# Kernel optimization log

Measured on AMD Instinct MI355X. Metric: run time of the kernel, lower is better.

## Reference

```python
import jax, jax.numpy as jnp
import numpy as np

B, A, H, D, K = 131072, 6, 256, 128, 512
BETA = 0.25
VQ_LOSS_WEIGHT = 1.0


def setup_inputs() -> dict:
    key = jax.random.key(0)
    ks = jax.random.split(key, 16)
    s = 0.05
    inp = {
        "action": jax.random.normal(ks[0], (B, A), jnp.float32),
        # encoder: Linear(A,H)+ReLU, Linear(H,H)+ReLU, Linear(H,D)
        "enc1_w": jax.random.normal(ks[1], (H, A), jnp.float32) * s,
        "enc1_b": jnp.zeros((H,), jnp.float32),
        "enc2_w": jax.random.normal(ks[2], (H, H), jnp.float32) * s,
        "enc2_b": jnp.zeros((H,), jnp.float32),
        "mu_w": jax.random.normal(ks[3], (D, H), jnp.float32) * s,
        "mu_b": jnp.zeros((D,), jnp.float32),
        # VQ codebook, uniform(-1/K, 1/K) as in torch init
        "emb": jax.random.uniform(ks[4], (K, D), jnp.float32, -1.0 / K, 1.0 / K),
        # decoder: Linear(D,H)+ReLU, Linear(H,H)+ReLU, Linear(H,A)+Tanh
        "dec1_w": jax.random.normal(ks[5], (H, D), jnp.float32) * s,
        "dec1_b": jnp.zeros((H,), jnp.float32),
        "dec2_w": jax.random.normal(ks[6], (H, H), jnp.float32) * s,
        "dec2_b": jnp.zeros((H,), jnp.float32),
        "rec_w": jax.random.normal(ks[7], (A, H), jnp.float32) * s,
        "rec_b": jnp.zeros((A,), jnp.float32),
    }
    return inp


def _lin(x, w, b):
    return x @ w.T + b


def reference(action, enc1_w, enc1_b, enc2_w, enc2_b, mu_w, mu_b, emb,
              dec1_w, dec1_b, dec2_w, dec2_b, rec_w, rec_b):
    sg = jax.lax.stop_gradient
    # encoder MLP -> (B, D)
    h = jax.nn.relu(_lin(action, enc1_w, enc1_b))
    h = jax.nn.relu(_lin(h, enc2_w, enc2_b))
    enc = _lin(h, mu_w, mu_b)
    # VQ: argmin over squared L2 distance (same argmin as torch.cdist p=2)
    d2 = (jnp.sum(enc * enc, axis=1, keepdims=True)
          - 2.0 * (enc @ emb.T)
          + jnp.sum(emb * emb, axis=1))  # (B, K)
    idx = jnp.argmin(d2, axis=-1)  # (B,)
    q = emb[idx]  # (B, D) gather == onehot @ emb
    commitment_loss = jnp.mean((enc - sg(q)) ** 2)
    embedding_loss = jnp.mean((q - sg(enc)) ** 2)
    vq_loss = BETA * commitment_loss + embedding_loss
    # straight-through estimator
    q_st = enc + sg(q - enc)
    # decoder MLP (decode_action_head + decode_common + recons_action_head)
    h = jax.nn.relu(_lin(q_st, dec1_w, dec1_b))
    h = jax.nn.relu(_lin(h, dec2_w, dec2_b))
    recons = jnp.tanh(_lin(h, rec_w, rec_b))
    recons_loss = jnp.mean((recons - action) ** 2)
    total_loss = recons_loss + VQ_LOSS_WEIGHT * vq_loss
    return idx, q_st, total_loss
```

## Files before the change

### kernel.cpp

```cpp
#include <hip/hip_runtime.h>
#include <hip/hip_bf16.h>

#define NB 131072
#define MARGINF 5e-7f
#define WS_E2 256
#define WS_MASK 768
#define WS_MASKW 4096
#define WS_BASE_BYTES ((768 + 4096) * 4)
#define WS_SPLIT_F 4864
#define OFF_W2 0
#define OFF_W3 131072
#define OFF_EMB 196608
#define OFF_D1 327680
#define OFF_D2 393216
#define OFF_RW 524288
#define SPLIT_TOTAL 532480

typedef __attribute__((ext_vector_type(8))) short short8v;
typedef __attribute__((ext_vector_type(4))) float f32x4;
typedef __attribute__((ext_vector_type(4))) unsigned short ushort4v;

#define SWC(j) ((((j) >> 2) & 7) << 2)

__device__ __forceinline__ unsigned short bf16rn(float x) {
    unsigned u = __float_as_uint(x);
    unsigned r = u + 0x7fffu + ((u >> 16) & 1u);
    return (unsigned short)(r >> 16);
}
__device__ __forceinline__ void split2(float x, unsigned short& h, unsigned short& l) {
    h = bf16rn(x);
    float hf = __uint_as_float((unsigned)h << 16);
    l = bf16rn(x - hf);
}

__global__ void prep_kernel(
    const float* __restrict__ w2, const float* __restrict__ w3,
    const float* __restrict__ emb, const float* __restrict__ d1w,
    const float* __restrict__ d2w, const float* __restrict__ rw,
    float* __restrict__ ws, int do_splits)
{
    const int total = 512 + 266240;
    unsigned short* wsb = (unsigned short*)(ws + WS_SPLIT_F);
    for (int idx = blockIdx.x * 256 + threadIdx.x; idx < total; idx += gridDim.x * 256) {
        if (idx < 512) {
            const float* e = emb + (size_t)idx * 128;
            float s0 = 0.f, s1 = 0.f, s2 = 0.f, s3 = 0.f;
            for (int d = 0; d < 128; d += 4) {
                s0 += e[d] * e[d];     s1 += e[d + 1] * e[d + 1];
                s2 += e[d + 2] * e[d + 2]; s3 += e[d + 3] * e[d + 3];
            }
            ws[WS_E2 + idx] = (s0 + s1) + (s2 + s3);
            continue;
        }
        if (!do_splits) continue;
        int j = idx - 512;
        int base, K, o, k;
        float src;
        if (j < 65536) {
            o = j >> 8; k = j & 255; base = OFF_W2; K = 256; src = w2[o * 256 + k];
        } else if (j < 98304) {
            j -= 65536; o = j >> 8; k = j & 255; base = OFF_W3; K = 256; src = w3[o * 256 + k];
        } else if (j < 163840) {
            j -= 98304; o = j >> 7; k = j & 127; base = OFF_EMB; K = 128; src = emb[o * 128 + k];
        } else if (j < 196608) {
            j -= 163840; o = j >> 7; k = j & 127; base = OFF_D1; K = 128; src = d1w[o * 128 + k];
        } else if (j < 262144) {
            j -= 196608; o = j >> 8; k = j & 255; base = OFF_D2; K = 256; src = d2w[o * 256 + k];
        } else {
            j -= 262144; o = j >> 8; k = j & 255; base = OFF_RW; K = 256;
            src = (o < 6) ? rw[o * 256 + k] : 0.f;
        }
        unsigned short h, l;
        split2(src, h, l);
        int jt = o >> 4, c = k >> 5;
        int lane = (((k >> 3) & 3) << 4) | (o & 15);
        int e = k & 7;
        int a = base + ((jt * (K >> 5) + c) * 2) * 512 + lane * 8 + e;
        wsb[a] = h;
        wsb[a + 512] = l;
    }
}


template<int NJT, int KC, bool RELU, bool SQSUM, int TERMS, bool WRITELO>
__device__ __forceinline__ void mfma_mlp4(
    const short8v* __restrict__ Wf, const float* __restrict__ bias,
    unsigned short* HHp, unsigned short* HLp, float* ENC2Wp,
    int w, int lane)
{
    const int lc = lane & 15, lg = lane >> 4;
    f32x4 acc[NJT][4];
#pragma unroll
    for (int jj = 0; jj < NJT; ++jj)
#pragma unroll
        for (int rt = 0; rt < 4; ++rt)
            acc[jj][rt] = (f32x4){0.f, 0.f, 0.f, 0.f};

    __syncthreads();
    for (int c = 0; c < KC; ++c) {
        const int boff = c * 32 + lg * 8;
        short8v bh[4], bl[4];
#pragma unroll
        for (int rt = 0; rt < 4; ++rt) {
            bh[rt] = *(const short8v*)&HHp[(rt * 16 + lc) * 264 + boff];
            if (TERMS == 3)
                bl[rt] = *(const short8v*)&HLp[(rt * 16 + lc) * 264 + boff];
        }
#pragma unroll
        for (int jj = 0; jj < NJT; ++jj) {
            int fi = (((w * NJT + jj) * KC + c) * 2) * 64 + lane;
            short8v ah = Wf[fi];
            if (TERMS == 3) {
                short8v al = Wf[fi + 64];
#pragma unroll
                for (int rt = 0; rt < 4; ++rt) {
                    acc[jj][rt] = __builtin_amdgcn_mfma_f32_16x16x32_bf16(al, bh[rt], acc[jj][rt], 0, 0, 0);
                    acc[jj][rt] = __builtin_amdgcn_mfma_f32_16x16x32_bf16(ah, bl[rt], acc[jj][rt], 0, 0, 0);
                    acc[jj][rt] = __builtin_amdgcn_mfma_f32_16x16x32_bf16(ah, bh[rt], acc[jj][rt], 0, 0, 0);
                }
            } else {
#pragma unroll
                for (int rt = 0; rt < 4; ++rt)
                    acc[jj][rt] = __builtin_amdgcn_mfma_f32_16x16x32_bf16(ah, bh[rt], acc[jj][rt], 0, 0, 0);
            }
        }
    }
    __syncthreads();

    float sq[4] = {0.f, 0.f, 0.f, 0.f};
#pragma unroll
    for (int jj = 0; jj < NJT; ++jj) {
        int j0 = (w * NJT + jj) * 16 + lg * 4;
        float4 bv = *(const float4*)&bias[j0];
        float bb[4] = {bv.x, bv.y, bv.z, bv.w};
#pragma unroll
        for (int rt = 0; rt < 4; ++rt) {
            int r = rt * 16 + lc;
            ushort4v hv, lv;
#pragma unroll
            for (int reg = 0; reg < 4; ++reg) {
                float v = acc[jj][rt][reg] + bb[reg];
                if (RELU) v = fmaxf(v, 0.f);
                if (SQSUM) sq[rt] += v * v;
                if (WRITELO) {
                    unsigned short h, l;
                    split2(v, h, l);
                    hv[reg] = h; lv[reg] = l;
                } else {
                    hv[reg] = bf16rn(v);
                }
            }
            *(ushort4v*)&HHp[r * 264 + j0] = hv;
            if (WRITELO) *(ushort4v*)&HLp[r * 264 + j0] = lv;
        }
    }
    if (SQSUM) {
#pragma unroll
        for (int rt = 0; rt < 4; ++rt) {
            float s = sq[rt];
            s += __shfl_xor(s, 16);
            s += __shfl_xor(s, 32);
            if (lg == 0) ENC2Wp[w * 64 + rt * 16 + lc] = s;
        }
    }
}

__global__ __launch_bounds__(256, 2) void vqvae_main_mfma(
    const float* __restrict__ action,
    const float* __restrict__ w1, const float* __restrict__ b1,
    const float* __restrict__ b2, const float* __restrict__ b3,
    const float* __restrict__ emb,
    const float* __restrict__ d1b, const float* __restrict__ d2b,
    const float* __restrict__ rb,
    float* __restrict__ out, float* __restrict__ ws)
{
    extern __shared__ __align__(16) unsigned short DYN[];
    unsigned short* HH = DYN;
    unsigned short* HL = DYN + 64 * 264;

    __shared__ float AT[64 * 6];
    __shared__ float E2S[512];
    __shared__ float TOPV[4][64][3];
    __shared__ float ENC2W[4 * 64];
    __shared__ int IDXR[64];
    __shared__ int FLAGR[64];
    __shared__ float RED[8];

    const int t = threadIdx.x;
    const int w = t >> 6, lane = t & 63;
    const int lc = lane & 15, lg = lane >> 4;
    const int row0 = blockIdx.x * 64;
    const unsigned short* wsb = (const unsigned short*)(ws + WS_SPLIT_F);
    const short8v* W2f = (const short8v*)wsb + OFF_W2 / 8;
    const short8v* W3f = (const short8v*)wsb + OFF_W3 / 8;
    const short8v* EMBf = (const short8v*)wsb + OFF_EMB / 8;
    const short8v* D1f = (const short8v*)wsb + OFF_D1 / 8;
    const short8v* D2f = (const short8v*)wsb + OFF_D2 / 8;
    const short8v* RWf = (const short8v*)wsb + OFF_RW / 8;

    for (int i = t; i < 384; i += 256) AT[i] = action[(size_t)row0 * 6 + i];
    for (int i = t; i < 512; i += 256) E2S[i] = ws[WS_E2 + i];
    __syncthreads();

    {
        float wr[6];
#pragma unroll
        for (int i = 0; i < 6; ++i) wr[i] = w1[t * 6 + i];
        float bb = b1[t];
        for (int r = 0; r < 64; ++r) {
            float s = bb;
#pragma unroll
            for (int i = 0; i < 6; ++i) s += wr[i] * AT[r * 6 + i];
            s = fmaxf(s, 0.f);
            unsigned short h, l;
            split2(s, h, l);
            HH[r * 264 + t] = h;
            HL[r * 264 + t] = l;
        }
    }

    mfma_mlp4<4, 8, true, false, 3, true>(W2f, b2, HH, HL, ENC2W, w, lane);
    mfma_mlp4<2, 8, false, true, 3, true>(W3f, b3, HH, HL, ENC2W, w, lane);

    float lvq = 0.f, lrec = 0.f;
    {
        float v1[4][4], v2[4][4];
        int k1r[4][4];
#pragma unroll
        for (int rt = 0; rt < 4; ++rt)
#pragma unroll
            for (int reg = 0; reg < 4; ++reg) {
                v1[rt][reg] = 1e30f; v2[rt][reg] = 1e30f; k1r[rt][reg] = 0;
            }
        __syncthreads();
#pragma unroll
        for (int p = 0; p < 2; ++p) {
            f32x4 vacc[4][4];
#pragma unroll
            for (int kt = 0; kt < 4; ++kt)
#pragma unroll
                for (int rt = 0; rt < 4; ++rt)
                    vacc[kt][rt] = (f32x4){0.f, 0.f, 0.f, 0.f};
            for (int c = 0; c < 4; ++c) {
                const int aoff = c * 32 + lg * 8;
                short8v ah[4], al[4];
#pragma unroll
                for (int rt = 0; rt < 4; ++rt) {
                    ah[rt] = *(const short8v*)&HH[(rt * 16 + lc) * 264 + aoff];
                    al[rt] = *(const short8v*)&HL[(rt * 16 + lc) * 264 + aoff];
                }
#pragma unroll
                for (int kt = 0; kt < 4; ++kt) {
                    int ktg = w * 8 + p * 4 + kt;
                    int fi = ((ktg * 4 + c) * 2) * 64 + lane;
                    short8v bh = EMBf[fi];
                    short8v bl = EMBf[fi + 64];
#pragma unroll
                    for (int rt = 0; rt < 4; ++rt) {
                        vacc[kt][rt] = __builtin_amdgcn_mfma_f32_16x16x32_bf16(al[rt], bh, vacc[kt][rt], 0, 0, 0);
                        vacc[kt][rt] = __builtin_amdgcn_mfma_f32_16x16x32_bf16(ah[rt], bl, vacc[kt][rt], 0, 0, 0);
                        vacc[kt][rt] = __builtin_amdgcn_mfma_f32_16x16x32_bf16(ah[rt], bh, vacc[kt][rt], 0, 0, 0);
                    }
                }
            }
#pragma unroll
            for (int kt = 0; kt < 4; ++kt) {
                int k = (w * 8 + p * 4 + kt) * 16 + lc;
                float ek = E2S[k];
#pragma unroll
                for (int rt = 0; rt < 4; ++rt)
#pragma unroll
                    for (int reg = 0; reg < 4; ++reg) {
                        float dd = ek - 2.f * vacc[kt][rt][reg];
                        if (dd < v1[rt][reg]) {
                            v2[rt][reg] = v1[rt][reg]; v1[rt][reg] = dd; k1r[rt][reg] = k;
                        } else if (dd < v2[rt][reg]) v2[rt][reg] = dd;
                    }
            }
        }
        __syncthreads();

#pragma unroll
        for (int m = 1; m < 16; m <<= 1) {
#pragma unroll
            for (int rt = 0; rt < 4; ++rt)
#pragma unroll
                for (int reg = 0; reg < 4; ++reg) {
                    float ov1 = __shfl_xor(v1[rt][reg], m);
                    int ok1 = __shfl_xor(k1r[rt][reg], m);
                    float ov2 = __shfl_xor(v2[rt][reg], m);
                    if (ov1 < v1[rt][reg] ||
                        (ov1 == v1[rt][reg] && ok1 < k1r[rt][reg])) {
                        v2[rt][reg] = fminf(v1[rt][reg], ov2);
                        v1[rt][reg] = ov1; k1r[rt][reg] = ok1;
                    } else {
                        v2[rt][reg] = fminf(v2[rt][reg], ov1);
                    }
                }
        }
        if (lc == 0) {
#pragma unroll
            for (int rt = 0; rt < 4; ++rt)
#pragma unroll
                for (int reg = 0; reg < 4; ++reg) {
                    int row = rt * 16 + lg * 4 + reg;
                    TOPV[w][row][0] = v1[rt][reg];
                    TOPV[w][row][1] = __int_as_float(k1r[rt][reg]);
                    TOPV[w][row][2] = v2[rt][reg];
                }
        }
    }
    __syncthreads();

    if (t < 64) {
        float v1 = 1e30f, v2 = 1e30f; int k1 = 0;
#pragma unroll
        for (int ww = 0; ww < 4; ++ww) {
            float ov1 = TOPV[ww][t][0];
            int ok1 = __float_as_int(TOPV[ww][t][1]);
            float ov2 = TOPV[ww][t][2];
            if (ov1 < v1 || (ov1 == v1 && ok1 < k1)) {
                v2 = fminf(v1, ov2); v1 = ov1; k1 = ok1;
            } else {
                v2 = fminf(v2, ov1);
            }
        }
        int flag = (v2 - v1 >= MARGINF) ? 0 : 1;
        IDXR[t] = k1;
        FLAGR[t] = flag;
        int row = row0 + t;
        if (flag)
            atomicOr((unsigned int*)ws + WS_MASK + (row >> 5), 1u << (row & 31));
        out[row] = (float)k1;
        if (!flag) {
            float enc2 = ENC2W[0 * 64 + t] + ENC2W[1 * 64 + t] +
                         ENC2W[2 * 64 + t] + ENC2W[3 * 64 + t];
            lvq = enc2 + v1;
        }
    }
    __syncthreads();

    {
        int d = t & 127, rhalf = t >> 7;
#pragma unroll
        for (int e = 0; e < 32; ++e) {
            int r = (e << 1) | rhalf;
            int k1 = IDXR[r];
            float q = emb[(size_t)k1 * 128 + d];
            out[NB + (size_t)(row0 + r) * 128 + d] = q;
            HH[r * 264 + d] = bf16rn(q);
        }
    }

    mfma_mlp4<4, 4, true, false, 1, false>(D1f, d1b, HH, HL, ENC2W, w, lane);
    mfma_mlp4<4, 8, true, false, 1, false>(D2f, d2b, HH, HL, ENC2W, w, lane);
    __syncthreads();

    {
        f32x4 racc = (f32x4){0.f, 0.f, 0.f, 0.f};
        for (int c = 0; c < 8; ++c) {
            const int boff = c * 32 + lg * 8;
            short8v bh = *(const short8v*)&HH[(w * 16 + lc) * 264 + boff];
            int fi = (c * 2) * 64 + lane;
            short8v ah = RWf[fi];
            racc = __builtin_amdgcn_mfma_f32_16x16x32_bf16(ah, bh, racc, 0, 0, 0);
        }
        int r = w * 16 + lc;
#pragma unroll
        for (int reg = 0; reg < 4; ++reg) {
            int j = lg * 4 + reg;
            if (j < 6) {
                float rec = tanhf(racc[reg] + rb[j]);
                float df = rec - AT[r * 6 + j];
                if (!FLAGR[r]) lrec += df * df;
            }
        }
    }

#pragma unroll
    for (int m = 1; m < 64; m <<= 1) {
        lvq += __shfl_xor(lvq, m);
        lrec += __shfl_xor(lrec, m);
    }
    if ((t & 63) == 0) { RED[t >> 6] = lvq; RED[4 + (t >> 6)] = lrec; }
    __syncthreads();
    if (t == 0) {
        int slot = blockIdx.x & 63;
        atomicAdd((double*)ws + slot, (double)((RED[0] + RED[1]) + (RED[2] + RED[3])));
        atomicAdd((double*)ws + 64 + slot, (double)((RED[4] + RED[5]) + (RED[6] + RED[7])));
    }
}

__global__ __launch_bounds__(256) void vqvae_fix(
    const float* __restrict__ action,
    const float* __restrict__ w1, const float* __restrict__ b1,
    const float* __restrict__ w2, const float* __restrict__ b2,
    const float* __restrict__ w3, const float* __restrict__ b3,
    const float* __restrict__ emb,
    const float* __restrict__ d1w, const float* __restrict__ d1b,
    const float* __restrict__ d2w, const float* __restrict__ d2b,
    const float* __restrict__ rw, const float* __restrict__ rb,
    float* __restrict__ out, float* __restrict__ ws)
{
    __shared__ double H1[256];
    __shared__ double H2[256];
    __shared__ double ENC[128];
    __shared__ double QD[128];
    __shared__ double SRED[256];
    __shared__ int SK[256];
    __shared__ double SA[6];

    const int t = threadIdx.x;

    for (int widx = blockIdx.x; widx < WS_MASKW; widx += gridDim.x) {
        const unsigned int word = ((const unsigned int*)ws)[WS_MASK + widx];
        if (word == 0u) continue;

        for (int bit = 0; bit < 32; ++bit) {
            if (!(word & (1u << bit))) continue;
            const int row = (widx << 5) + bit;

            if (t < 6) SA[t] = (double)action[(size_t)row * 6 + t];
            __syncthreads();
            {
                double a = (double)b1[t];
#pragma unroll
                for (int i = 0; i < 6; ++i) a += (double)w1[t * 6 + i] * SA[i];
                H1[t] = a > 0.0 ? a : 0.0;
            }
            __syncthreads();
            {
                const float* w = w2 + (size_t)t * 256;
                double a0 = 0, a1 = 0, a2 = 0, a3 = 0;
                for (int i = 0; i < 256; i += 4) {
                    a0 += (double)w[i] * H1[i];     a1 += (double)w[i + 1] * H1[i + 1];
                    a2 += (double)w[i + 2] * H1[i + 2]; a3 += (double)w[i + 3] * H1[i + 3];
                }
                double a = (double)b2[t] + a0 + a1 + a2 + a3;
                H2[t] = a > 0.0 ? a : 0.0;
            }
            __syncthreads();
            if (t < 128) {
                const float* w = w3 + (size_t)t * 256;
                double a0 = 0, a1 = 0, a2 = 0, a3 = 0;
                for (int i = 0; i < 256; i += 4) {
                    a0 += (double)w[i] * H2[i];     a1 += (double)w[i + 1] * H2[i + 1];
                    a2 += (double)w[i + 2] * H2[i + 2]; a3 += (double)w[i + 3] * H2[i + 3];
                }
                ENC[t] = (double)b3[t] + a0 + a1 + a2 + a3;
            }
            __syncthreads();
            double best = 1e300; int bk = 0;
#pragma unroll
            for (int kk = 0; kk < 2; ++kk) {
                int k = t + kk * 256;
                const float* e = emb + (size_t)k * 128;
                double s0 = 0, s1 = 0;
                for (int d = 0; d < 128; d += 2) {
                    double df0 = ENC[d] - (double)e[d];
                    double df1 = ENC[d + 1] - (double)e[d + 1];
                    s0 += df0 * df0; s1 += df1 * df1;
                }
                double s = s0 + s1;
                if (s < best) { best = s; bk = k; }
            }
            SRED[t] = best; SK[t] = bk;
            __syncthreads();
            for (int st = 128; st > 0; st >>= 1) {
                if (t < st) {
                    double ov = SRED[t + st]; int ok = SK[t + st];
                    if (ov < SRED[t] || (ov == SRED[t] && ok < SK[t])) { SRED[t] = ov; SK[t] = ok; }
                }
                __syncthreads();
            }
            const int bestk = SK[0];
            double lv = 0.0;
            if (t < 128) {
                double q = (double)emb[(size_t)bestk * 128 + t];
                QD[t] = q;
                double df = ENC[t] - q;
                lv = df * df;
                out[NB + (size_t)row * 128 + t] = (float)q;
            }
            if (t == 0) out[row] = (float)bestk;
            __syncthreads();
            {
                const float* w = d1w + (size_t)t * 128;
                double a0 = 0, a1 = 0;
                for (int i = 0; i < 128; i += 2) {
                    a0 += (double)w[i] * QD[i]; a1 += (double)w[i + 1] * QD[i + 1];
                }
                double a = (double)d1b[t] + a0 + a1;
                H1[t] = a > 0.0 ? a : 0.0;
            }
            __syncthreads();
            {
                const float* w = d2w + (size_t)t * 256;
                double a0 = 0, a1 = 0, a2 = 0, a3 = 0;
                for (int i = 0; i < 256; i += 4) {
                    a0 += (double)w[i] * H1[i];     a1 += (double)w[i + 1] * H1[i + 1];
                    a2 += (double)w[i + 2] * H1[i + 2]; a3 += (double)w[i + 3] * H1[i + 3];
                }
                double a = (double)d2b[t] + a0 + a1 + a2 + a3;
                H2[t] = a > 0.0 ? a : 0.0;
            }
            __syncthreads();
            double lr = 0.0;
            if (t < 6) {
                const float* w = rw + (size_t)t * 256;
                double a0 = 0, a1 = 0;
                for (int i = 0; i < 256; i += 2) {
                    a0 += (double)w[i] * H2[i]; a1 += (double)w[i + 1] * H2[i + 1];
                }
                double rec = tanh((double)rb[t] + a0 + a1);
                double df = rec - SA[t];
                lr = df * df;
            }
            SRED[t] = lv;
            __syncthreads();
            for (int st = 128; st > 0; st >>= 1) {
                if (t < st) SRED[t] += SRED[t + st];
                __syncthreads();
            }
            if (t == 0) atomicAdd((double*)ws + 0, SRED[0]);
            if (t < 6) atomicAdd((double*)ws + 64, lr);
            __syncthreads();
        }
    }
}

__global__ void vqvae_fin(const float* __restrict__ ws, float* __restrict__ out) {
    if (threadIdx.x == 0 && blockIdx.x == 0) {
        const double* D = (const double*)ws;
        double sv = 0.0, sr = 0.0;
        for (int i = 0; i < 64; ++i) { sv += D[i]; sr += D[64 + i]; }
        double loss = sr / ((double)NB * 6.0) + 1.25 * (sv / ((double)NB * 128.0));
        out[(size_t)NB * 129] = (float)loss;
    }
}

static __device__ __forceinline__ void gemm_out256(
    const float* __restrict__ W, const float* __restrict__ bias, int IN,
    const float* __restrict__ hin, float* __restrict__ hout,
    float* __restrict__ WC, int t, int tx, int r0, bool do_relu)
{
    float acc[2][4][4];
#pragma unroll
    for (int g = 0; g < 2; ++g)
#pragma unroll
        for (int a = 0; a < 4; ++a)
#pragma unroll
            for (int b = 0; b < 4; ++b) acc[g][a][b] = 0.f;
    float4 pa = *(const float4*)(W + (size_t)t * IN);
    float4 pb = *(const float4*)(W + (size_t)t * IN + 4);
    for (int i0 = 0; i0 < IN; i0 += 8) {
        __syncthreads();
        WC[0 * 256 + t] = pa.x; WC[1 * 256 + t] = pa.y;
        WC[2 * 256 + t] = pa.z; WC[3 * 256 + t] = pa.w;
        WC[4 * 256 + t] = pb.x; WC[5 * 256 + t] = pb.y;
        WC[6 * 256 + t] = pb.z; WC[7 * 256 + t] = pb.w;
        __syncthreads();
        if (i0 + 8 < IN) {
            pa = *(const float4*)(W + (size_t)t * IN + i0 + 8);
            pb = *(const float4*)(W + (size_t)t * IN + i0 + 12);
        }
#pragma unroll
        for (int i = 0; i < 8; ++i) {
            int row = i0 + i;
            float4 h = *(const float4*)&hin[row * 32 + (r0 ^ SWC(row))];
            float4 w0 = *(const float4*)&WC[i * 256 + 4 * tx];
            float4 w1v = *(const float4*)&WC[i * 256 + 128 + 4 * tx];
            float wv0[4] = {w0.x, w0.y, w0.z, w0.w};
            float wv1[4] = {w1v.x, w1v.y, w1v.z, w1v.w};
            float hv[4] = {h.x, h.y, h.z, h.w};
#pragma unroll
            for (int a = 0; a < 4; ++a)
#pragma unroll
                for (int b = 0; b < 4; ++b) {
                    acc[0][a][b] += wv0[a] * hv[b];
                    acc[1][a][b] += wv1[a] * hv[b];
                }
        }
    }
#pragma unroll
    for (int g = 0; g < 2; ++g)
#pragma unroll
        for (int a = 0; a < 4; ++a) {
            int j = g * 128 + 4 * tx + a;
            float bj = bias[j];
            float4 v;
            v.x = acc[g][a][0] + bj; v.y = acc[g][a][1] + bj;
            v.z = acc[g][a][2] + bj; v.w = acc[g][a][3] + bj;
            if (do_relu) {
                v.x = fmaxf(v.x, 0.f); v.y = fmaxf(v.y, 0.f);
                v.z = fmaxf(v.z, 0.f); v.w = fmaxf(v.w, 0.f);
            }
            *(float4*)&hout[j * 32 + (r0 ^ SWC(j))] = v;
        }
    __syncthreads();
}

__global__ __launch_bounds__(256, 2) void vqvae_main_fp32(
    const float* __restrict__ action,
    const float* __restrict__ w1, const float* __restrict__ b1,
    const float* __restrict__ w2, const float* __restrict__ b2,
    const float* __restrict__ w3, const float* __restrict__ b3,
    const float* __restrict__ emb,
    const float* __restrict__ d1w, const float* __restrict__ d1b,
    const float* __restrict__ d2w, const float* __restrict__ d2b,
    const float* __restrict__ rw, const float* __restrict__ rb,
    float* __restrict__ out, float* __restrict__ ws)
{
    __shared__ float X[256 * 32];
    __shared__ float Y[256 * 32];
    __shared__ float WC[2048];
    __shared__ float AT[6 * 32];
    __shared__ int IDXR[32];
    __shared__ int FLAGR[32];
    __shared__ float RED[8];

    const int t = threadIdx.x;
    const int tx = t & 31, ty = t >> 5;
    const int r0 = ty * 4;
    const int row0 = blockIdx.x * 32;

    if (t < 192) {
        int r = t / 6, i = t - r * 6;
        AT[i * 32 + r] = action[(size_t)row0 * 6 + t];
    }
    __syncthreads();
    {
#pragma unroll
        for (int i = 0; i < 6; ++i) WC[i * 256 + t] = w1[t * 6 + i];
        __syncthreads();
        float acc[2][4][4];
#pragma unroll
        for (int g = 0; g < 2; ++g)
#pragma unroll
            for (int a = 0; a < 4; ++a)
#pragma unroll
                for (int b = 0; b < 4; ++b) acc[g][a][b] = 0.f;
#pragma unroll
        for (int i = 0; i < 6; ++i) {
            float4 h = *(const float4*)&AT[i * 32 + r0];
            float4 w0 = *(const float4*)&WC[i * 256 + 4 * tx];
            float4 w1v = *(const float4*)&WC[i * 256 + 128 + 4 * tx];
            float wv0[4] = {w0.x, w0.y, w0.z, w0.w};
            float wv1[4] = {w1v.x, w1v.y, w1v.z, w1v.w};
            float hv[4] = {h.x, h.y, h.z, h.w};
#pragma unroll
            for (int a = 0; a < 4; ++a)
#pragma unroll
                for (int b = 0; b < 4; ++b) {
                    acc[0][a][b] += wv0[a] * hv[b];
                    acc[1][a][b] += wv1[a] * hv[b];
                }
        }
#pragma unroll
        for (int g = 0; g < 2; ++g)
#pragma unroll
            for (int a = 0; a < 4; ++a) {
                int j = g * 128 + 4 * tx + a;
                float bj = b1[j];
                float4 v;
                v.x = fmaxf(acc[g][a][0] + bj, 0.f);
                v.y = fmaxf(acc[g][a][1] + bj, 0.f);
                v.z = fmaxf(acc[g][a][2] + bj, 0.f);
                v.w = fmaxf(acc[g][a][3] + bj, 0.f);
                *(float4*)&X[j * 32 + (r0 ^ SWC(j))] = v;
            }
        __syncthreads();
    }
    gemm_out256(w2, b2, 256, X, Y, WC, t, tx, r0, true);
    {
        float acc[4][4];
#pragma unroll
        for (int a = 0; a < 4; ++a)
#pragma unroll
            for (int b = 0; b < 4; ++b) acc[a][b] = 0.f;
        float4 pa, pb;
        if (t < 128) {
            pa = *(const float4*)(w3 + (size_t)t * 256);
            pb = *(const float4*)(w3 + (size_t)t * 256 + 4);
        }
        for (int i0 = 0; i0 < 256; i0 += 8) {
            __syncthreads();
            if (t < 128) {
                WC[0 * 128 + t] = pa.x; WC[1 * 128 + t] = pa.y;
                WC[2 * 128 + t] = pa.z; WC[3 * 128 + t] = pa.w;
                WC[4 * 128 + t] = pb.x; WC[5 * 128 + t] = pb.y;
                WC[6 * 128 + t] = pb.z; WC[7 * 128 + t] = pb.w;
            }
            __syncthreads();
            if (t < 128 && i0 + 8 < 256) {
                pa = *(const float4*)(w3 + (size_t)t * 256 + i0 + 8);
                pb = *(const float4*)(w3 + (size_t)t * 256 + i0 + 12);
            }
#pragma unroll
            for (int i = 0; i < 8; ++i) {
                int row = i0 + i;
                float4 h = *(const float4*)&Y[row * 32 + (r0 ^ SWC(row))];
                float4 w0 = *(const float4*)&WC[i * 128 + 4 * tx];
                float wv[4] = {w0.x, w0.y, w0.z, w0.w};
                float hv[4] = {h.x, h.y, h.z, h.w};
#pragma unroll
                for (int a = 0; a < 4; ++a)
#pragma unroll
                    for (int b = 0; b < 4; ++b) acc[a][b] += wv[a] * hv[b];
            }
        }
#pragma unroll
        for (int a = 0; a < 4; ++a) {
            int j = 4 * tx + a;
            float bj = b3[j];
            float4 v;
            v.x = acc[a][0] + bj; v.y = acc[a][1] + bj;
            v.z = acc[a][2] + bj; v.w = acc[a][3] + bj;
            *(float4*)&X[j * 32 + (r0 ^ SWC(j))] = v;
        }
        __syncthreads();
    }
    {
        float bv1[4], bv2[4];
        int bk1[4];
        float acc[4][4][4];
#pragma unroll
        for (int p = 0; p < 4; ++p)
#pragma unroll
            for (int a = 0; a < 4; ++a)
#pragma unroll
                for (int b = 0; b < 4; ++b) acc[p][a][b] = 0.f;
        float4 qa = *(const float4*)(emb + (size_t)t * 128);
        float4 qb = *(const float4*)(emb + (size_t)(t + 256) * 128);
        for (int d0 = 0; d0 < 128; d0 += 4) {
            __syncthreads();
            WC[0 * 512 + t] = qa.x; WC[1 * 512 + t] = qa.y;
            WC[2 * 512 + t] = qa.z; WC[3 * 512 + t] = qa.w;
            WC[0 * 512 + 256 + t] = qb.x; WC[1 * 512 + 256 + t] = qb.y;
            WC[2 * 512 + 256 + t] = qb.z; WC[3 * 512 + 256 + t] = qb.w;
            __syncthreads();
            if (d0 + 4 < 128) {
                qa = *(const float4*)(emb + (size_t)t * 128 + d0 + 4);
                qb = *(const float4*)(emb + (size_t)(t + 256) * 128 + d0 + 4);
            }
#pragma unroll
            for (int i = 0; i < 4; ++i) {
                int row = d0 + i;
                float4 h = *(const float4*)&X[row * 32 + (r0 ^ SWC(row))];
                float hv[4] = {h.x, h.y, h.z, h.w};
#pragma unroll
                for (int p = 0; p < 4; ++p) {
                    float4 w0 = *(const float4*)&WC[i * 512 + p * 128 + 4 * tx];
                    float wv[4] = {w0.x, w0.y, w0.z, w0.w};
#pragma unroll
                    for (int a = 0; a < 4; ++a)
#pragma unroll
                        for (int b = 0; b < 4; ++b) acc[p][a][b] += wv[a] * hv[b];
                }
            }
        }
#pragma unroll
        for (int b = 0; b < 4; ++b) { bv1[b] = 1e30f; bv2[b] = 1e30f; bk1[b] = 0; }
#pragma unroll
        for (int p = 0; p < 4; ++p)
#pragma unroll
            for (int a = 0; a < 4; ++a) {
                int k = p * 128 + 4 * tx + a;
                float ek = ws[WS_E2 + k];
#pragma unroll
                for (int b = 0; b < 4; ++b) {
                    float dd = ek - 2.f * acc[p][a][b];
                    if (dd < bv1[b]) { bv2[b] = bv1[b]; bv1[b] = dd; bk1[b] = k; }
                    else if (dd < bv2[b]) bv2[b] = dd;
                }
            }
#pragma unroll
        for (int m = 1; m < 32; m <<= 1) {
#pragma unroll
            for (int b = 0; b < 4; ++b) {
                float ov1 = __shfl_xor(bv1[b], m);
                int ok1 = __shfl_xor(bk1[b], m);
                float ov2 = __shfl_xor(bv2[b], m);
                if (ov1 < bv1[b] || (ov1 == bv1[b] && ok1 < bk1[b])) {
                    bv2[b] = fminf(bv1[b], ov2);
                    bv1[b] = ov1; bk1[b] = ok1;
                } else {
                    bv2[b] = fminf(bv2[b], ov1);
                }
            }
        }
        if (tx == 0) {
#pragma unroll
            for (int b = 0; b < 4; ++b) {
                IDXR[r0 + b] = bk1[b];
                FLAGR[r0 + b] = (bv2[b] - bv1[b] >= MARGINF) ? 0 : 1;
            }
        }
    }
    __syncthreads();
    if (t < 32) {
        int row = row0 + t;
        if (FLAGR[t])
            atomicOr((unsigned int*)ws + WS_MASK + (row >> 5), 1u << (row & 31));
        out[row] = (float)IDXR[t];
    }
    float lvq = 0.f, lrec = 0.f;
    {
        int d = t & 127, rq = t >> 7;
        int cd = SWC(d);
#pragma unroll
        for (int e = 0; e < 4; ++e) {
            int rr = (rq + 2 * e) * 4;
            float4 en = *(const float4*)&X[d * 32 + (rr ^ cd)];
            float q0 = emb[(size_t)IDXR[rr + 0] * 128 + d];
            float q1 = emb[(size_t)IDXR[rr + 1] * 128 + d];
            float q2 = emb[(size_t)IDXR[rr + 2] * 128 + d];
            float q3 = emb[(size_t)IDXR[rr + 3] * 128 + d];
            float4 qv; qv.x = q0; qv.y = q1; qv.z = q2; qv.w = q3;
            *(float4*)&X[(128 + d) * 32 + (rr ^ cd)] = qv;
            if (!FLAGR[rr + 0]) lvq += (en.x - q0) * (en.x - q0);
            if (!FLAGR[rr + 1]) lvq += (en.y - q1) * (en.y - q1);
            if (!FLAGR[rr + 2]) lvq += (en.z - q2) * (en.z - q2);
            if (!FLAGR[rr + 3]) lvq += (en.w - q3) * (en.w - q3);
            out[NB + (size_t)(row0 + rr + 0) * 128 + d] = q0;
            out[NB + (size_t)(row0 + rr + 1) * 128 + d] = q1;
            out[NB + (size_t)(row0 + rr + 2) * 128 + d] = q2;
            out[NB + (size_t)(row0 + rr + 3) * 128 + d] = q3;
        }
    }
    __syncthreads();
    gemm_out256(d1w, d1b, 128, X + 128 * 32, Y, WC, t, tx, r0, true);
    gemm_out256(d2w, d2b, 256, Y, X, WC, t, tx, r0, true);
    if (t < 192) {
        int jj = t >> 5, r = t & 31;
        const float* wr = rw + jj * 256;
        float a0 = 0.f, a1 = 0.f, a2 = 0.f, a3 = 0.f;
        for (int i = 0; i < 256; i += 4) {
            a0 += wr[i] * X[i * 32 + (r ^ SWC(i))];
            a1 += wr[i + 1] * X[(i + 1) * 32 + (r ^ SWC(i + 1))];
            a2 += wr[i + 2] * X[(i + 2) * 32 + (r ^ SWC(i + 2))];
            a3 += wr[i + 3] * X[(i + 3) * 32 + (r ^ SWC(i + 3))];
        }
        float rec = tanhf(rb[jj] + (a0 + a1) + (a2 + a3));
        float df = rec - AT[jj * 32 + r];
        if (!FLAGR[r]) lrec = df * df;
    }
#pragma unroll
    for (int m = 1; m < 64; m <<= 1) {
        lvq += __shfl_xor(lvq, m);
        lrec += __shfl_xor(lrec, m);
    }
    if ((t & 63) == 0) { RED[t >> 6] = lvq; RED[4 + (t >> 6)] = lrec; }
    __syncthreads();
    if (t == 0) {
        int slot = blockIdx.x & 63;
        atomicAdd((double*)ws + slot, (double)((RED[0] + RED[1]) + (RED[2] + RED[3])));
        atomicAdd((double*)ws + 64 + slot, (double)((RED[4] + RED[5]) + (RED[6] + RED[7])));
    }
}

extern "C" void kernel_launch(void* const* d_in, const int* in_sizes, int n_in,
                              void* d_out, int out_size, void* d_ws, size_t ws_size,
                              hipStream_t stream) {
    const float* action = (const float*)d_in[0];
    const float* w1 = (const float*)d_in[1];
    const float* b1 = (const float*)d_in[2];
    const float* w2 = (const float*)d_in[3];
    const float* b2 = (const float*)d_in[4];
    const float* w3 = (const float*)d_in[5];
    const float* b3 = (const float*)d_in[6];
    const float* emb = (const float*)d_in[7];
    const float* d1w = (const float*)d_in[8];
    const float* d1b = (const float*)d_in[9];
    const float* d2w = (const float*)d_in[10];
    const float* d2b = (const float*)d_in[11];
    const float* rw = (const float*)d_in[12];
    const float* rb = (const float*)d_in[13];
    float* out = (float*)d_out;
    float* ws = (float*)d_ws;

    const size_t need_mfma = (size_t)WS_BASE_BYTES + (size_t)SPLIT_TOTAL * 2;
    const int use_mfma = (ws_size >= need_mfma) ? 1 : 0;
    const int dyn_lds = 64 * 264 * 2 * 2;

    size_t clear = ws_size < (size_t)WS_BASE_BYTES ? ws_size : (size_t)WS_BASE_BYTES;
    hipMemsetAsync(d_ws, 0, clear, stream);

    prep_kernel<<<1043, 256, 0, stream>>>(w2, w3, emb, d1w, d2w, rw, ws, use_mfma);
    if (use_mfma) {
        hipFuncSetAttribute((const void*)vqvae_main_mfma,
                            hipFuncAttributeMaxDynamicSharedMemorySize, dyn_lds);
        vqvae_main_mfma<<<NB / 64, 256, dyn_lds, stream>>>(action, w1, b1, b2, b3, emb,
                                                           d1b, d2b, rb, out, ws);
    } else {
        vqvae_main_fp32<<<NB / 32, 256, 0, stream>>>(action, w1, b1, w2, b2, w3, b3, emb,
                                                     d1w, d1b, d2w, d2b, rw, rb, out, ws);
    }
    vqvae_fix<<<256, 256, 0, stream>>>(action, w1, b1, w2, b2, w3, b3, emb,
                                       d1w, d1b, d2w, d2b, rw, rb, out, ws);
    vqvae_fin<<<1, 64, 0, stream>>>(ws, out);
}
```

Baseline: 395.6 us.

## Use single-bf16 VQ distance screening with exact fp32 candidate rescoring

Replaces the 3-term split-bf16 MFMA distance computation with a single bf16 hi*hi pass. Each row takes a coarse minimum, and every code within a margin of it is marked as a candidate in an LDS bitmask. Candidates are then rescored exactly in fp32 by one thread per row, which yields the argmin and the second-best margin. It also drops the low-half weight writes for matrices that no longer need them and moves the workspace clearing from a memset into the prep kernel. The gain is a third of the MFMA work in the VQ stage, paid for with serial per-row rescoring whose cost grows with the candidate count, plus an accuracy risk if the coarse margin is too tight.

```diff
diff --git a/kernel.cpp b/kernel.cpp
--- a/kernel.cpp
+++ b/kernel.cpp
@@ -3,6 +3,7 @@
 
 #define NB 131072
 #define MARGINF 5e-7f
+#define CMARGINF 4e-4f
 #define WS_E2 256
 #define WS_MASK 768
 #define WS_MASKW 4096
@@ -39,9 +40,15 @@
     const float* __restrict__ d2w, const float* __restrict__ rw,
     float* __restrict__ ws, int do_splits)
 {
+    const int gid = blockIdx.x * 256 + threadIdx.x;
+    const int stride = gridDim.x * 256;
+    for (int z = gid; z < 4352; z += stride) {
+        int a = (z < 256) ? z : (512 + z);
+        ws[a] = 0.f;
+    }
     const int total = 512 + 266240;
     unsigned short* wsb = (unsigned short*)(ws + WS_SPLIT_F);
-    for (int idx = blockIdx.x * 256 + threadIdx.x; idx < total; idx += gridDim.x * 256) {
+    for (int idx = gid; idx < total; idx += stride) {
         if (idx < 512) {
             const float* e = emb + (size_t)idx * 128;
             float s0 = 0.f, s1 = 0.f, s2 = 0.f, s3 = 0.f;
@@ -56,19 +63,20 @@
         int j = idx - 512;
         int base, K, o, k;
         float src;
+        bool wlo;
         if (j < 65536) {
-            o = j >> 8; k = j & 255; base = OFF_W2; K = 256; src = w2[o * 256 + k];
+            o = j >> 8; k = j & 255; base = OFF_W2; K = 256; src = w2[o * 256 + k]; wlo = true;
         } else if (j < 98304) {
-            j -= 65536; o = j >> 8; k = j & 255; base = OFF_W3; K = 256; src = w3[o * 256 + k];
+            j -= 65536; o = j >> 8; k = j & 255; base = OFF_W3; K = 256; src = w3[o * 256 + k]; wlo = true;
         } else if (j < 163840) {
-            j -= 98304; o = j >> 7; k = j & 127; base = OFF_EMB; K = 128; src = emb[o * 128 + k];
+            j -= 98304; o = j >> 7; k = j & 127; base = OFF_EMB; K = 128; src = emb[o * 128 + k]; wlo = false;
         } else if (j < 196608) {
-            j -= 163840; o = j >> 7; k = j & 127; base = OFF_D1; K = 128; src = d1w[o * 128 + k];
+            j -= 163840; o = j >> 7; k = j & 127; base = OFF_D1; K = 128; src = d1w[o * 128 + k]; wlo = false;
         } else if (j < 262144) {
-            j -= 196608; o = j >> 8; k = j & 255; base = OFF_D2; K = 256; src = d2w[o * 256 + k];
+            j -= 196608; o = j >> 8; k = j & 255; base = OFF_D2; K = 256; src = d2w[o * 256 + k]; wlo = false;
         } else {
             j -= 262144; o = j >> 8; k = j & 255; base = OFF_RW; K = 256;
-            src = (o < 6) ? rw[o * 256 + k] : 0.f;
+            src = (o < 6) ? rw[o * 256 + k] : 0.f; wlo = false;
         }
         unsigned short h, l;
         split2(src, h, l);
@@ -77,7 +85,7 @@
         int e = k & 7;
         int a = base + ((jt * (K >> 5) + c) * 2) * 512 + lane * 8 + e;
         wsb[a] = h;
-        wsb[a + 512] = l;
+        if (wlo) wsb[a + 512] = l;
     }
 }
 
@@ -180,8 +188,10 @@
 
     __shared__ float AT[64 * 6];
     __shared__ float E2S[512];
-    __shared__ float TOPV[4][64][3];
     __shared__ float ENC2W[4 * 64];
+    __shared__ float WMIN[4][64];
+    __shared__ float CMIN[64];
+    __shared__ unsigned int CAND[64 * 16];
     __shared__ int IDXR[64];
     __shared__ int FLAGR[64];
     __shared__ float RED[8];
@@ -224,117 +234,114 @@
 
     float lvq = 0.f, lrec = 0.f;
     {
-        float v1[4][4], v2[4][4];
-        int k1r[4][4];
+        for (int i = t; i < 1024; i += 256) CAND[i] = 0u;
+        f32x4 vacc[8][4];
+#pragma unroll
+        for (int kt = 0; kt < 8; ++kt)
+#pragma unroll
+            for (int rt = 0; rt < 4; ++rt)
+                vacc[kt][rt] = (f32x4){0.f, 0.f, 0.f, 0.f};
+        __syncthreads();
+        for (int c = 0; c < 4; ++c) {
+            const int aoff = c * 32 + lg * 8;
+            short8v ah[4];
+#pragma unroll
+            for (int rt = 0; rt < 4; ++rt)
+                ah[rt] = *(const short8v*)&HH[(rt * 16 + lc) * 264 + aoff];
+#pragma unroll
+            for (int kt = 0; kt < 8; ++kt) {
+                int fi = (((w * 8 + kt) * 4 + c) * 2) * 64 + lane;
+                short8v bh = EMBf[fi];
+#pragma unroll
+                for (int rt = 0; rt < 4; ++rt)
+                    vacc[kt][rt] = __builtin_amdgcn_mfma_f32_16x16x32_bf16(ah[rt], bh, vacc[kt][rt], 0, 0, 0);
+            }
+        }
+        float v1[4][4];
 #pragma unroll
         for (int rt = 0; rt < 4; ++rt)
 #pragma unroll
-            for (int reg = 0; reg < 4; ++reg) {
-                v1[rt][reg] = 1e30f; v2[rt][reg] = 1e30f; k1r[rt][reg] = 0;
-            }
+            for (int reg = 0; reg < 4; ++reg) v1[rt][reg] = 1e30f;
+#pragma unroll
+        for (int kt = 0; kt < 8; ++kt) {
+            int k = (w * 8 + kt) * 16 + lc;
+            float ek = E2S[k];
+#pragma unroll
+            for (int rt = 0; rt < 4; ++rt)
+#pragma unroll
+                for (int reg = 0; reg < 4; ++reg) {
+                    float dd = ek - 2.f * vacc[kt][rt][reg];
+                    v1[rt][reg] = fminf(v1[rt][reg], dd);
+                }
+        }
+#pragma unroll
+        for (int m = 1; m < 16; m <<= 1)
+#pragma unroll
+            for (int rt = 0; rt < 4; ++rt)
+#pragma unroll
+                for (int reg = 0; reg < 4; ++reg)
+                    v1[rt][reg] = fminf(v1[rt][reg], __shfl_xor(v1[rt][reg], m));
+        if (lc == 0) {
+#pragma unroll
+            for (int rt = 0; rt < 4; ++rt)
+#pragma unroll
+                for (int reg = 0; reg < 4; ++reg)
+                    WMIN[w][rt * 16 + lg * 4 + reg] = v1[rt][reg];
+        }
         __syncthreads();
-#pragma unroll
-        for (int p = 0; p < 2; ++p) {
-            f32x4 vacc[4][4];
-#pragma unroll
-            for (int kt = 0; kt < 4; ++kt)
-#pragma unroll
-                for (int rt = 0; rt < 4; ++rt)
-                    vacc[kt][rt] = (f32x4){0.f, 0.f, 0.f, 0.f};
-            for (int c = 0; c < 4; ++c) {
-                const int aoff = c * 32 + lg * 8;
-                short8v ah[4], al[4];
-#pragma unroll
-                for (int rt = 0; rt < 4; ++rt) {
-                    ah[rt] = *(const short8v*)&HH[(rt * 16 + lc) * 264 + aoff];
-                    al[rt] = *(const short8v*)&HL[(rt * 16 + lc) * 264 + aoff];
-                }
-#pragma unroll
-                for (int kt = 0; kt < 4; ++kt) {
-                    int ktg = w * 8 + p * 4 + kt;
-                    int fi = ((ktg * 4 + c) * 2) * 64 + lane;
-                    short8v bh = EMBf[fi];
-                    short8v bl = EMBf[fi + 64];
-#pragma unroll
-                    for (int rt = 0; rt < 4; ++rt) {
-                        vacc[kt][rt] = __builtin_amdgcn_mfma_f32_16x16x32_bf16(al[rt], bh, vacc[kt][rt], 0, 0, 0);
-                        vacc[kt][rt] = __builtin_amdgcn_mfma_f32_16x16x32_bf16(ah[rt], bl, vacc[kt][rt], 0, 0, 0);
-                        vacc[kt][rt] = __builtin_amdgcn_mfma_f32_16x16x32_bf16(ah[rt], bh, vacc[kt][rt], 0, 0, 0);
-                    }
-                }
-            }
-#pragma unroll
-            for (int kt = 0; kt < 4; ++kt) {
-                int k = (w * 8 + p * 4 + kt) * 16 + lc;
-                float ek = E2S[k];
-#pragma unroll
-                for (int rt = 0; rt < 4; ++rt)
-#pragma unroll
-                    for (int reg = 0; reg < 4; ++reg) {
-                        float dd = ek - 2.f * vacc[kt][rt][reg];
-                        if (dd < v1[rt][reg]) {
-                            v2[rt][reg] = v1[rt][reg]; v1[rt][reg] = dd; k1r[rt][reg] = k;
-                        } else if (dd < v2[rt][reg]) v2[rt][reg] = dd;
-                    }
-            }
-        }
+        if (t < 64)
+            CMIN[t] = fminf(fminf(WMIN[0][t], WMIN[1][t]), fminf(WMIN[2][t], WMIN[3][t]));
         __syncthreads();
-
-#pragma unroll
-        for (int m = 1; m < 16; m <<= 1) {
-#pragma unroll
-            for (int rt = 0; rt < 4; ++rt)
-#pragma unroll
-                for (int reg = 0; reg < 4; ++reg) {
-                    float ov1 = __shfl_xor(v1[rt][reg], m);
-                    int ok1 = __shfl_xor(k1r[rt][reg], m);
-                    float ov2 = __shfl_xor(v2[rt][reg], m);
-                    if (ov1 < v1[rt][reg] ||
-                        (ov1 == v1[rt][reg] && ok1 < k1r[rt][reg])) {
-                        v2[rt][reg] = fminf(v1[rt][reg], ov2);
-                        v1[rt][reg] = ov1; k1r[rt][reg] = ok1;
-                    } else {
-                        v2[rt][reg] = fminf(v2[rt][reg], ov1);
-                    }
-                }
-        }
-        if (lc == 0) {
+#pragma unroll
+        for (int kt = 0; kt < 8; ++kt) {
+            int k = (w * 8 + kt) * 16 + lc;
+            float ek = E2S[k];
 #pragma unroll
             for (int rt = 0; rt < 4; ++rt)
 #pragma unroll
                 for (int reg = 0; reg < 4; ++reg) {
                     int row = rt * 16 + lg * 4 + reg;
-                    TOPV[w][row][0] = v1[rt][reg];
-                    TOPV[w][row][1] = __int_as_float(k1r[rt][reg]);
-                    TOPV[w][row][2] = v2[rt][reg];
+                    float dd = ek - 2.f * vacc[kt][rt][reg];
+                    if (!(dd > CMIN[row] + CMARGINF))
+                        atomicOr(&CAND[row * 16 + (k >> 5)], 1u << (k & 31));
                 }
         }
     }
     __syncthreads();
 
     if (t < 64) {
+        const int row = t;
         float v1 = 1e30f, v2 = 1e30f; int k1 = 0;
-#pragma unroll
-        for (int ww = 0; ww < 4; ++ww) {
-            float ov1 = TOPV[ww][t][0];
-            int ok1 = __float_as_int(TOPV[ww][t][1]);
-            float ov2 = TOPV[ww][t][2];
-            if (ov1 < v1 || (ov1 == v1 && ok1 < k1)) {
-                v2 = fminf(v1, ov2); v1 = ov1; k1 = ok1;
-            } else {
-                v2 = fminf(v2, ov1);
+        for (int wd = 0; wd < 16; ++wd) {
+            unsigned int m = CAND[row * 16 + wd];
+            while (m) {
+                int b = __ffs(m) - 1; m &= m - 1;
+                int k = wd * 32 + b;
+                const float* ek = emb + (size_t)k * 128;
+                float s0 = 0.f, s1 = 0.f;
+                for (int d = 0; d < 128; d += 2) {
+                    float e0 = __uint_as_float((unsigned)HH[row * 264 + d] << 16)
+                             + __uint_as_float((unsigned)HL[row * 264 + d] << 16);
+                    float e1 = __uint_as_float((unsigned)HH[row * 264 + d + 1] << 16)
+                             + __uint_as_float((unsigned)HL[row * 264 + d + 1] << 16);
+                    s0 += e0 * ek[d];
+                    s1 += e1 * ek[d + 1];
+                }
+                float dd = E2S[k] - 2.f * (s0 + s1);
+                if (dd < v1) { v2 = v1; v1 = dd; k1 = k; }
+                else if (dd < v2) v2 = dd;
             }
         }
         int flag = (v2 - v1 >= MARGINF) ? 0 : 1;
-        IDXR[t] = k1;
-        FLAGR[t] = flag;
-        int row = row0 + t;
+        IDXR[row] = k1;
+        FLAGR[row] = flag;
+        int grow = row0 + row;
         if (flag)
-            atomicOr((unsigned int*)ws + WS_MASK + (row >> 5), 1u << (row & 31));
-        out[row] = (float)k1;
+            atomicOr((unsigned int*)ws + WS_MASK + (grow >> 5), 1u << (grow & 31));
+        out[grow] = (float)k1;
         if (!flag) {
-            float enc2 = ENC2W[0 * 64 + t] + ENC2W[1 * 64 + t] +
-                         ENC2W[2 * 64 + t] + ENC2W[3 * 64 + t];
+            float enc2 = ENC2W[0 * 64 + row] + ENC2W[1 * 64 + row] +
+                         ENC2W[2 * 64 + row] + ENC2W[3 * 64 + row];
             lvq = enc2 + v1;
         }
     }
@@ -883,9 +890,6 @@
     const int use_mfma = (ws_size >= need_mfma) ? 1 : 0;
     const int dyn_lds = 64 * 264 * 2 * 2;
 
-    size_t clear = ws_size < (size_t)WS_BASE_BYTES ? ws_size : (size_t)WS_BASE_BYTES;
-    hipMemsetAsync(d_ws, 0, clear, stream);
-
     prep_kernel<<<1043, 256, 0, stream>>>(w2, w3, emb, d1w, d2w, rw, ws, use_mfma);
     if (use_mfma) {
         hipFuncSetAttribute((const void*)vqvae_main_mfma,
```

Result: slower. 1.414 ms (+257.3%).
